# Performance work log

Hardware: AMD Instinct MI355X
Metric: run time of the kernel (lower is better)

## Reference

```python
import jax, jax.numpy as jnp
import numpy as np

N = 50000          # nodes
E = 1_600_000      # edges (avg degree 32)
IN = 128           # in_channels
H = 2              # heads
C = 64             # out_channels per head


def setup_inputs() -> dict:
    key = jax.random.key(0)
    k = jax.random.split(key, 6)
    x = jax.random.normal(k[0], (N, IN), dtype=jnp.float32)
    edge_index = jax.random.randint(k[1], (2, E), 0, N, dtype=jnp.int32)
    W = jax.random.normal(k[2], (IN, H * C), dtype=jnp.float32) / np.sqrt(IN).astype(np.float32)
    att_src = jax.random.normal(k[3], (H, C), dtype=jnp.float32) * 0.1
    att_dst = jax.random.normal(k[4], (H, C), dtype=jnp.float32) * 0.1
    bias = jnp.zeros((C,), dtype=jnp.float32)
    return {"x": x, "W": W, "att_src": att_src, "att_dst": att_dst,
            "bias": bias, "edge_index": edge_index}


def reference(x, W, att_src, att_dst, bias, edge_index):
    Nn = x.shape[0]
    # linear projection per head: [N, H, C]
    h = (x @ W).reshape(Nn, H, C)
    # PyG GATConv default: add self loops
    loops = jnp.arange(Nn, dtype=edge_index.dtype)
    src = jnp.concatenate([edge_index[0], loops])  # [E+N]
    dst = jnp.concatenate([edge_index[1], loops])
    # per-node attention logits: a_src . h, a_dst . h -> [N, H]
    a_s = jnp.sum(h * att_src, axis=-1)
    a_d = jnp.sum(h * att_dst, axis=-1)
    # per-edge score, leaky relu (slope 0.2)
    e = jax.nn.leaky_relu(a_s[src] + a_d[dst], 0.2)  # [E+N, H]
    # softmax over incoming edges per destination node
    emax = jax.lax.stop_gradient(jax.ops.segment_max(e, dst, num_segments=Nn))
    e = jnp.exp(e - emax[dst])
    esum = jax.ops.segment_sum(e, dst, num_segments=Nn)
    alpha = e / (esum[dst] + 1e-16)                  # [E+N, H]
    # attention-weighted message passing: scatter-sum to destinations
    out = jax.ops.segment_sum(h[src] * alpha[:, :, None], dst, num_segments=Nn)  # [N, H, C]
    # concat=False -> mean over heads, then bias
    return out.mean(axis=1) + bias  # [N, C]
```

## Files before the change

### kernel.cpp

```cpp
#include <hip/hip_runtime.h>
#include <hip/hip_bf16.h>


#define NBLK 256
#define TH 512
#define BSH 7
#define BSZ 128
#define MAXBUCK 512
#define PLCAP 8192

typedef __attribute__((ext_vector_type(8))) short bf16x8;
typedef __attribute__((ext_vector_type(4))) float f32x4;

__device__ __forceinline__ ushort f2bf(float f) {
  __hip_bfloat16 b = __float2bfloat16(f);
  union { __hip_bfloat16 b; ushort u; } cv; cv.b = b; return cv.u;
}
__device__ __forceinline__ uint pk2(float a, float b) {
  return (uint)f2bf(a) | ((uint)f2bf(b) << 16);
}

__global__ __launch_bounds__(128) void k_wa(const float* __restrict__ W,
                                            const float* __restrict__ as,
                                            const float* __restrict__ ad,
                                            ushort* __restrict__ wa) {
  const int k = threadIdx.x;
  float s0 = 0.f, s1 = 0.f, d0 = 0.f, d1 = 0.f;
  const float* wr = &W[k * 128];
  for (int c = 0; c < 64; ++c) {
    float w0 = wr[c], w1 = wr[64 + c];
    s0 = fmaf(w0, as[c], s0);
    s1 = fmaf(w1, as[64 + c], s1);
    d0 = fmaf(w0, ad[c], d0);
    d1 = fmaf(w1, ad[64 + c], d1);
  }
  wa[k * 4 + 0] = f2bf(s0);
  wa[k * 4 + 1] = f2bf(s1);
  wa[k * 4 + 2] = f2bf(d0);
  wa[k * 4 + 3] = f2bf(d1);
}

__global__ __launch_bounds__(256) void k_gemm(
    const float* __restrict__ x, const float* __restrict__ W,
    const ushort* __restrict__ wa, __hip_bfloat162* __restrict__ h2,
    float* __restrict__ a_s, float* __restrict__ a_d, int Nn) {
  __shared__ ushort Al[64 * 128];
  char* lb = (char*)Al;
  const int wave = threadIdx.x >> 6;
  const int lane = threadIdx.x & 63;
  const int row0 = blockIdx.x * 64;
  const int l15 = lane & 15;
  const int kb = (lane >> 4) * 8;

  {
    const int t = threadIdx.x;
    const int srow = t >> 2, q = t & 3;
    int gr = row0 + srow; gr = (gr < Nn) ? gr : (Nn - 1);
    const float4* xr = (const float4*)&x[(size_t)gr * 128 + q * 32];
#pragma unroll
    for (int i = 0; i < 4; ++i) {
      float4 v0 = xr[2 * i], v1 = xr[2 * i + 1];
      uint4 w;
      w.x = pk2(v0.x, v0.y); w.y = pk2(v0.z, v0.w);
      w.z = pk2(v1.x, v1.y); w.w = pk2(v1.z, v1.w);
      int byte = srow * 256 + ((q * 64 + i * 16) ^ ((srow & 7) << 4));
      *(uint4*)(lb + byte) = w;
    }
  }

  bf16x8 bfr[2][4];
#pragma unroll
  for (int c = 0; c < 2; ++c) {
#pragma unroll
    for (int ks = 0; ks < 4; ++ks) {
      const float* wp = &W[(ks * 32 + kb) * 128 + wave * 32 + c * 16 + l15];
      union { bf16x8 v; ushort u[8]; } t;
#pragma unroll
      for (int j = 0; j < 8; ++j) t.u[j] = f2bf(wp[j * 128]);
      bfr[c][ks] = t.v;
    }
  }
  bf16x8 wafr[4];
  if (wave == 3) {
#pragma unroll
    for (int ks = 0; ks < 4; ++ks) {
      union { bf16x8 v; ushort u[8]; } t;
#pragma unroll
      for (int j = 0; j < 8; ++j)
        t.u[j] = (l15 < 4) ? wa[(ks * 32 + kb + j) * 4 + l15] : (ushort)0;
      wafr[ks] = t.v;
    }
  }

  __syncthreads();

  f32x4 acc[4][2];
  f32x4 accwa[4];
#pragma unroll
  for (int r = 0; r < 4; ++r) {
    acc[r][0] = (f32x4){0.f, 0.f, 0.f, 0.f};
    acc[r][1] = (f32x4){0.f, 0.f, 0.f, 0.f};
    accwa[r] = (f32x4){0.f, 0.f, 0.f, 0.f};
  }
#pragma unroll
  for (int ks = 0; ks < 4; ++ks) {
    bf16x8 af[4];
#pragma unroll
    for (int r = 0; r < 4; ++r) {
      int row = r * 16 + l15;
      int byte = row * 256 + ((ks * 64 + (lane >> 4) * 16) ^ ((row & 7) << 4));
      uint4 v = *(const uint4*)(lb + byte);
      union { uint4 q; bf16x8 v; } cv; cv.q = v;
      af[r] = cv.v;
    }
#pragma unroll
    for (int r = 0; r < 4; ++r) {
      acc[r][0] = __builtin_amdgcn_mfma_f32_16x16x32_bf16(af[r], bfr[0][ks],
                                                          acc[r][0], 0, 0, 0);
      acc[r][1] = __builtin_amdgcn_mfma_f32_16x16x32_bf16(af[r], bfr[1][ks],
                                                          acc[r][1], 0, 0, 0);
    }
    if (wave == 3) {
#pragma unroll
      for (int r = 0; r < 4; ++r)
        accwa[r] = __builtin_amdgcn_mfma_f32_16x16x32_bf16(af[r], wafr[ks],
                                                           accwa[r], 0, 0, 0);
    }
  }

  ushort* hs = (ushort*)h2;
  const int rbase = (lane >> 4) * 4;
#pragma unroll
  for (int r = 0; r < 4; ++r) {
#pragma unroll
    for (int c = 0; c < 2; ++c) {
      int col = wave * 32 + c * 16 + l15;
#pragma unroll
      for (int i = 0; i < 4; ++i) {
        int grow = row0 + r * 16 + rbase + i;
        if (grow < Nn) hs[(size_t)grow * 128 + col] = f2bf(acc[r][c][i]);
      }
    }
  }
  if (wave == 3) {
#pragma unroll
    for (int r = 0; r < 4; ++r) {
#pragma unroll
      for (int i = 0; i < 4; ++i) {
        int grow = row0 + r * 16 + rbase + i;
        if (grow < Nn) {
          float v = accwa[r][i];
          if (l15 < 2) a_s[grow * 2 + l15] = v;
          else if (l15 < 4) a_d[grow * 2 + (l15 - 2)] = v;
        }
      }
    }
  }
}

__global__ __launch_bounds__(TH) void k_bhist(const int* __restrict__ dst,
                                              int* __restrict__ bhist, int E,
                                              int nbuck, int chunk) {
  __shared__ int hl[MAXBUCK];
  for (int i = threadIdx.x; i < nbuck; i += TH) hl[i] = 0;
  __syncthreads();
  const int s = blockIdx.x * chunk;
  const int e = (s + chunk < E) ? s + chunk : E;
  for (int i = s + threadIdx.x; i < e; i += TH)
    atomicAdd(&hl[dst[i] >> BSH], 1);
  __syncthreads();
  for (int b = threadIdx.x; b < nbuck; b += TH)
    bhist[b * NBLK + blockIdx.x] = hl[b];
}

__global__ __launch_bounds__(NBLK) void k_bscan(const int* __restrict__ bhist,
                                                int* __restrict__ cursors,
                                                int* __restrict__ totals,
                                                int nbuck) {
  __shared__ int tmp[NBLK];
  const int b = blockIdx.x;
  const int t = threadIdx.x;
  const int v = bhist[b * NBLK + t];
  tmp[t] = v;
  __syncthreads();
  for (int d = 1; d < NBLK; d <<= 1) {
    int add = (t >= d) ? tmp[t - d] : 0;
    __syncthreads();
    tmp[t] += add;
    __syncthreads();
  }
  cursors[t * nbuck + b] = tmp[t] - v;
  if (t == NBLK - 1) totals[b] = tmp[t];
}

__global__ __launch_bounds__(MAXBUCK) void k_bbase(const int* __restrict__ totals,
                                                   int* __restrict__ bases,
                                                   int nbuck) {
  __shared__ int tmp[MAXBUCK];
  const int t = threadIdx.x;
  const int v = (t < nbuck) ? totals[t] : 0;
  tmp[t] = v;
  __syncthreads();
  for (int d = 1; d < MAXBUCK; d <<= 1) {
    int add = (t >= d) ? tmp[t - d] : 0;
    __syncthreads();
    tmp[t] += add;
    __syncthreads();
  }
  if (t < nbuck) bases[t] = tmp[t] - v;
  if (t == nbuck - 1) bases[nbuck] = tmp[t];
}

__global__ __launch_bounds__(TH) void k_binsert(
    const int* __restrict__ src, const int* __restrict__ dst,
    const int* __restrict__ cursors, const int* __restrict__ bases,
    int* __restrict__ pairs, int E, int nbuck, int chunk) {
  __shared__ int cur[MAXBUCK];
  for (int i = threadIdx.x; i < nbuck; i += TH)
    cur[i] = cursors[blockIdx.x * nbuck + i] + bases[i];
  __syncthreads();
  const int s = blockIdx.x * chunk;
  const int e = (s + chunk < E) ? s + chunk : E;
  for (int i = s + threadIdx.x; i < e; i += TH) {
    const int d = dst[i];
    const int b = d >> BSH;
    const int p = atomicAdd(&cur[b], 1);
    pairs[p] = ((d & (BSZ - 1)) << 16) | src[i];
  }
}

__global__ __launch_bounds__(256) void k_bucket(
    const int* __restrict__ pairs, const int* __restrict__ bases,
    int* __restrict__ off, int* __restrict__ cnt, int* __restrict__ csr,
    int Nn) {
  __shared__ int pl[PLCAP];
  __shared__ int cl[BSZ];
  __shared__ int tmp[BSZ];
  __shared__ int cu[BSZ];
  const int b = blockIdx.x;
  const int t = threadIdx.x;
  const int n0 = b << BSH;
  if (t < BSZ) cl[t] = 0;
  __syncthreads();
  const int s = bases[b], e = bases[b + 1];
  const int len = e - s;
  const bool fit = (len <= PLCAP);
  if (fit) {
    for (int i = t; i < len; i += 256) {
      int pv = pairs[s + i];
      pl[i] = pv;
      atomicAdd(&cl[pv >> 16], 1);
    }
  } else {
    for (int i = s + t; i < e; i += 256) atomicAdd(&cl[pairs[i] >> 16], 1);
  }
  __syncthreads();
  int v = 0;
  if (t < BSZ) { v = cl[t]; tmp[t] = v; }
  __syncthreads();
  for (int d = 1; d < BSZ; d <<= 1) {
    int add = (t < BSZ && t >= d) ? tmp[t - d] : 0;
    __syncthreads();
    if (t < BSZ) tmp[t] += add;
    __syncthreads();
  }
  if (t < BSZ) {
    const int excl = tmp[t] - v;
    cu[t] = s + excl;
    const int node = n0 + t;
    if (node < Nn) { off[node] = s + excl; cnt[node] = v; }
  }
  __syncthreads();
  if (fit) {
    for (int i = t; i < len; i += 256) {
      const int pv = pl[i];
      const int p = atomicAdd(&cu[pv >> 16], 1);
      csr[p] = pv & 0xffff;
    }
  } else {
    for (int i = s + t; i < e; i += 256) {
      const int pv = pairs[i];
      const int p = atomicAdd(&cu[pv >> 16], 1);
      csr[p] = pv & 0xffff;
    }
  }
}

__device__ __forceinline__ float leaky02(float v) {
  return fmaxf(v, 0.2f * v);
}

__global__ __launch_bounds__(256) void k_aggr(
    const __hip_bfloat162* __restrict__ h2, const float* __restrict__ a_s,
    const float* __restrict__ a_d, const int* __restrict__ off,
    const int* __restrict__ cnt, const int* __restrict__ csr,
    const float* __restrict__ bias, float* __restrict__ out, int Nn) {
  __shared__ uint2 ewA[4][64];
  __shared__ uint2 ewB[4][64];
  const int wave = threadIdx.x >> 6;
  const int lane = threadIdx.x & 63;
  const int d = blockIdx.x * 4 + wave;
  if (d >= Nn) return;
  const int o = off[d];
  const int deg = cnt[d];
  const float2 ad2 = *(const float2*)&a_d[d * 2];
  const char* hb = (const char*)h2;
  const unsigned l4 = lane * 4u;
  const uint4* ebase = (lane < 32) ? (const uint4*)&ewA[wave][0]
                                   : (const uint4*)&ewB[wave][0];

  float acc0 = 0.f, acc1 = 0.f;
  float sw0 = 0.f, sw1 = 0.f;

  for (int c = 0; c < deg; c += 64) {
    int rem = deg - c; if (rem > 64) rem = 64;
    {
      unsigned voff = 0; float w0 = 0.f, w1 = 0.f;
      if (lane < rem) {
        int sl = csr[o + c + lane];
        float2 as2 = *(const float2*)&a_s[sl * 2];
        w0 = __expf(leaky02(as2.x + ad2.x));
        w1 = __expf(leaky02(as2.y + ad2.y));
        voff = (unsigned)sl << 8;
        sw0 += w0; sw1 += w1;
      }
      ewA[wave][lane] = make_uint2(voff, __float_as_uint(w0));
      ewB[wave][lane] = make_uint2(voff, __float_as_uint(w1));
    }
    const int nq = (rem + 1) >> 1;
    int q = 0;
    for (; q + 4 <= nq; q += 4) {
      uint4 p0 = ebase[q + 0];
      uint4 p1 = ebase[q + 1];
      uint4 p2 = ebase[q + 2];
      uint4 p3 = ebase[q + 3];
      __hip_bfloat162 hA0 = *(const __hip_bfloat162*)(hb + (size_t)(p0.x + l4));
      __hip_bfloat162 hB0 = *(const __hip_bfloat162*)(hb + (size_t)(p0.z + l4));
      __hip_bfloat162 hA1 = *(const __hip_bfloat162*)(hb + (size_t)(p1.x + l4));
      __hip_bfloat162 hB1 = *(const __hip_bfloat162*)(hb + (size_t)(p1.z + l4));
      __hip_bfloat162 hA2 = *(const __hip_bfloat162*)(hb + (size_t)(p2.x + l4));
      __hip_bfloat162 hB2 = *(const __hip_bfloat162*)(hb + (size_t)(p2.z + l4));
      __hip_bfloat162 hA3 = *(const __hip_bfloat162*)(hb + (size_t)(p3.x + l4));
      __hip_bfloat162 hB3 = *(const __hip_bfloat162*)(hb + (size_t)(p3.z + l4));
      acc0 = fmaf(__uint_as_float(p0.y), __bfloat162float(hA0.x), acc0);
      acc1 = fmaf(__uint_as_float(p0.y), __bfloat162float(hA0.y), acc1);
      acc0 = fmaf(__uint_as_float(p0.w), __bfloat162float(hB0.x), acc0);
      acc1 = fmaf(__uint_as_float(p0.w), __bfloat162float(hB0.y), acc1);
      acc0 = fmaf(__uint_as_float(p1.y), __bfloat162float(hA1.x), acc0);
      acc1 = fmaf(__uint_as_float(p1.y), __bfloat162float(hA1.y), acc1);
      acc0 = fmaf(__uint_as_float(p1.w), __bfloat162float(hB1.x), acc0);
      acc1 = fmaf(__uint_as_float(p1.w), __bfloat162float(hB1.y), acc1);
      acc0 = fmaf(__uint_as_float(p2.y), __bfloat162float(hA2.x), acc0);
      acc1 = fmaf(__uint_as_float(p2.y), __bfloat162float(hA2.y), acc1);
      acc0 = fmaf(__uint_as_float(p2.w), __bfloat162float(hB2.x), acc0);
      acc1 = fmaf(__uint_as_float(p2.w), __bfloat162float(hB2.y), acc1);
      acc0 = fmaf(__uint_as_float(p3.y), __bfloat162float(hA3.x), acc0);
      acc1 = fmaf(__uint_as_float(p3.y), __bfloat162float(hA3.y), acc1);
      acc0 = fmaf(__uint_as_float(p3.w), __bfloat162float(hB3.x), acc0);
      acc1 = fmaf(__uint_as_float(p3.w), __bfloat162float(hB3.y), acc1);
    }
    for (; q < nq; ++q) {
      uint4 p = ebase[q];
      __hip_bfloat162 hA = *(const __hip_bfloat162*)(hb + (size_t)(p.x + l4));
      __hip_bfloat162 hB = *(const __hip_bfloat162*)(hb + (size_t)(p.z + l4));
      acc0 = fmaf(__uint_as_float(p.y), __bfloat162float(hA.x), acc0);
      acc1 = fmaf(__uint_as_float(p.y), __bfloat162float(hA.y), acc1);
      acc0 = fmaf(__uint_as_float(p.w), __bfloat162float(hB.x), acc0);
      acc1 = fmaf(__uint_as_float(p.w), __bfloat162float(hB.y), acc1);
    }
  }
#pragma unroll
  for (int msk = 1; msk <= 32; msk <<= 1) {
    sw0 += __shfl_xor(sw0, msk, 64);
    sw1 += __shfl_xor(sw1, msk, 64);
  }
  {
    float2 as2 = *(const float2*)&a_s[d * 2];
    float w0 = __expf(leaky02(as2.x + ad2.x));
    float w1 = __expf(leaky02(as2.y + ad2.y));
    sw0 += w0; sw1 += w1;
    float av = (lane < 32) ? w0 : w1;
    __hip_bfloat162 hv = h2[(size_t)d * 64 + lane];
    acc0 = fmaf(av, __bfloat162float(hv.x), acc0);
    acc1 = fmaf(av, __bfloat162float(hv.y), acc1);
  }
  const float invsel = 1.f / (((lane < 32) ? sw0 : sw1) + 1e-16f);
  acc0 *= invsel; acc1 *= invsel;
  float o0 = acc0 + __shfl_down(acc0, 32, 64);
  float o1 = acc1 + __shfl_down(acc1, 32, 64);
  if (lane < 32) {
    int c = lane * 2;
    float2 res = make_float2(0.5f * o0 + bias[c], 0.5f * o1 + bias[c + 1]);
    *(float2*)&out[(size_t)d * 64 + c] = res;
  }
}

extern "C" void kernel_launch(void* const* d_in, const int* in_sizes, int n_in,
                              void* d_out, int out_size, void* d_ws,
                              size_t ws_size, hipStream_t stream) {
  const float* x = (const float*)d_in[0];
  const float* W = (const float*)d_in[1];
  const float* att_s = (const float*)d_in[2];
  const float* att_d = (const float*)d_in[3];
  const float* bias = (const float*)d_in[4];
  const int* ei = (const int*)d_in[5];
  const int Nn = in_sizes[0] / 128;
  const int E = in_sizes[5] / 2;
  const int* src = ei;
  const int* dst = ei + E;
  float* out = (float*)d_out;

  const int nbuck = (Nn + BSZ - 1) >> BSH;
  const int chunk = (E + NBLK - 1) / NBLK;

  __hip_bfloat162* h2 = (__hip_bfloat162*)d_ws;
  float* a_s = (float*)(h2 + (size_t)Nn * 64);
  float* a_d = a_s + (size_t)Nn * 2;
  int* off = (int*)(a_d + (size_t)Nn * 2);
  int* cnt = off + Nn;
  int* bhist = cnt + Nn;
  int* cursors = bhist + (size_t)nbuck * NBLK;
  int* totals = cursors + (size_t)NBLK * nbuck;
  int* bases = totals + nbuck;
  ushort* wa = (ushort*)(bases + nbuck + 1);
  int* pairs = (int*)(wa + 512);
  int* csr = pairs + (size_t)E;

  hipLaunchKernelGGL(k_wa, dim3(1), dim3(128), 0, stream, W, att_s, att_d, wa);
  hipLaunchKernelGGL(k_gemm, dim3((Nn + 63) / 64), dim3(256), 0, stream, x, W,
                     wa, h2, a_s, a_d, Nn);
  hipLaunchKernelGGL(k_bhist, dim3(NBLK), dim3(TH), 0, stream, dst, bhist, E,
                     nbuck, chunk);
  hipLaunchKernelGGL(k_bscan, dim3(nbuck), dim3(NBLK), 0, stream, bhist,
                     cursors, totals, nbuck);
  hipLaunchKernelGGL(k_bbase, dim3(1), dim3(MAXBUCK), 0, stream, totals, bases,
                     nbuck);
  hipLaunchKernelGGL(k_binsert, dim3(NBLK), dim3(TH), 0, stream, src, dst,
                     cursors, bases, pairs, E, nbuck, chunk);
  hipLaunchKernelGGL(k_bucket, dim3(nbuck), dim3(256), 0, stream, pairs, bases,
                     off, cnt, csr, Nn);
  hipLaunchKernelGGL(k_aggr, dim3((Nn + 3) / 4), dim3(256), 0, stream, h2, a_s,
                     a_d, off, cnt, csr, bias, out, Nn);
}
```

Baseline: 117.8 us.

## Fuse GEMM with dst histogram, compute logits in epilogue, two nodes per wave

Merges the projection GEMM and the destination-bucket histogram into one launch, with extra blocks doing the histogram, and drops the separate k_wa kernel. Attention logits are now computed in the GEMM epilogue from fp32 accumulators via shared-memory atomics instead of an extra MFMA on precomputed bf16 weights. The aggregation kernel processes two destination nodes per wave, interleaving their first chunk to expose more independent gathers, and unpacks bf16 with shifts. This removes two launches and raises memory-level parallelism in the gather, at the cost of LDS atomics and more register pressure.

```diff
diff --git a/kernel.cpp b/kernel.cpp
--- a/kernel.cpp
+++ b/kernel.cpp
@@ -19,38 +19,41 @@
 __device__ __forceinline__ uint pk2(float a, float b) {
   return (uint)f2bf(a) | ((uint)f2bf(b) << 16);
 }
-
-__global__ __launch_bounds__(128) void k_wa(const float* __restrict__ W,
-                                            const float* __restrict__ as,
-                                            const float* __restrict__ ad,
-                                            ushort* __restrict__ wa) {
-  const int k = threadIdx.x;
-  float s0 = 0.f, s1 = 0.f, d0 = 0.f, d1 = 0.f;
-  const float* wr = &W[k * 128];
-  for (int c = 0; c < 64; ++c) {
-    float w0 = wr[c], w1 = wr[64 + c];
-    s0 = fmaf(w0, as[c], s0);
-    s1 = fmaf(w1, as[64 + c], s1);
-    d0 = fmaf(w0, ad[c], d0);
-    d1 = fmaf(w1, ad[64 + c], d1);
-  }
-  wa[k * 4 + 0] = f2bf(s0);
-  wa[k * 4 + 1] = f2bf(s1);
-  wa[k * 4 + 2] = f2bf(d0);
-  wa[k * 4 + 3] = f2bf(d1);
-}
-
-__global__ __launch_bounds__(256) void k_gemm(
+__device__ __forceinline__ float leaky02(float v) {
+  return fmaxf(v, 0.2f * v);
+}
+
+__global__ __launch_bounds__(256) void k_mega1(
     const float* __restrict__ x, const float* __restrict__ W,
-    const ushort* __restrict__ wa, __hip_bfloat162* __restrict__ h2,
-    float* __restrict__ a_s, float* __restrict__ a_d, int Nn) {
-  __shared__ ushort Al[64 * 128];
+    const float* __restrict__ att_s, const float* __restrict__ att_d,
+    __hip_bfloat162* __restrict__ h2, float* __restrict__ a_s,
+    float* __restrict__ a_d, int Nn, const int* __restrict__ dst,
+    int* __restrict__ bhist, int E, int nbuck, int chunkE, int ngemm) {
+  __shared__ char smem[64 * 128 * 2 + 64 * 4 * 4];
+  if ((int)blockIdx.x >= ngemm) {
+    int* hl = (int*)smem;
+    const int bb = (int)blockIdx.x - ngemm;
+    for (int i = threadIdx.x; i < nbuck; i += 256) hl[i] = 0;
+    __syncthreads();
+    const int s = bb * chunkE;
+    const int e = (s + chunkE < E) ? s + chunkE : E;
+    for (int i = s + threadIdx.x; i < e; i += 256)
+      atomicAdd(&hl[dst[i] >> BSH], 1);
+    __syncthreads();
+    for (int b = threadIdx.x; b < nbuck; b += 256)
+      bhist[b * NBLK + bb] = hl[b];
+    return;
+  }
+  ushort* Al = (ushort*)smem;
+  float(*asd)[4] = (float(*)[4])(smem + 64 * 128 * 2);
   char* lb = (char*)Al;
   const int wave = threadIdx.x >> 6;
   const int lane = threadIdx.x & 63;
   const int row0 = blockIdx.x * 64;
   const int l15 = lane & 15;
   const int kb = (lane >> 4) * 8;
+
+  ((float*)asd)[threadIdx.x] = 0.f;
 
   {
     const int t = threadIdx.x;
@@ -67,7 +70,6 @@
       *(uint4*)(lb + byte) = w;
     }
   }
-
   bf16x8 bfr[2][4];
 #pragma unroll
   for (int c = 0; c < 2; ++c) {
@@ -80,27 +82,18 @@
       bfr[c][ks] = t.v;
     }
   }
-  bf16x8 wafr[4];
-  if (wave == 3) {
-#pragma unroll
-    for (int ks = 0; ks < 4; ++ks) {
-      union { bf16x8 v; ushort u[8]; } t;
-#pragma unroll
-      for (int j = 0; j < 8; ++j)
-        t.u[j] = (l15 < 4) ? wa[(ks * 32 + kb + j) * 4 + l15] : (ushort)0;
-      wafr[ks] = t.v;
-    }
-  }
+  const int col0 = wave * 32 + l15, col1 = col0 + 16;
+  const float as0c = att_s[col0], as1c = att_s[col1];
+  const float ad0c = att_d[col0], ad1c = att_d[col1];
+  const int head = wave >> 1;
 
   __syncthreads();
 
   f32x4 acc[4][2];
-  f32x4 accwa[4];
 #pragma unroll
   for (int r = 0; r < 4; ++r) {
     acc[r][0] = (f32x4){0.f, 0.f, 0.f, 0.f};
     acc[r][1] = (f32x4){0.f, 0.f, 0.f, 0.f};
-    accwa[r] = (f32x4){0.f, 0.f, 0.f, 0.f};
   }
 #pragma unroll
   for (int ks = 0; ks < 4; ++ks) {
@@ -120,12 +113,6 @@
       acc[r][1] = __builtin_amdgcn_mfma_f32_16x16x32_bf16(af[r], bfr[1][ks],
                                                           acc[r][1], 0, 0, 0);
     }
-    if (wave == 3) {
-#pragma unroll
-      for (int r = 0; r < 4; ++r)
-        accwa[r] = __builtin_amdgcn_mfma_f32_16x16x32_bf16(af[r], wafr[ks],
-                                                           accwa[r], 0, 0, 0);
-    }
   }
 
   ushort* hs = (ushort*)h2;
@@ -133,44 +120,26 @@
 #pragma unroll
   for (int r = 0; r < 4; ++r) {
 #pragma unroll
-    for (int c = 0; c < 2; ++c) {
-      int col = wave * 32 + c * 16 + l15;
-#pragma unroll
-      for (int i = 0; i < 4; ++i) {
-        int grow = row0 + r * 16 + rbase + i;
-        if (grow < Nn) hs[(size_t)grow * 128 + col] = f2bf(acc[r][c][i]);
+    for (int i = 0; i < 4; ++i) {
+      const int lrow = r * 16 + rbase + i;
+      const int grow = row0 + lrow;
+      const float h0 = acc[r][0][i], h1 = acc[r][1][i];
+      if (grow < Nn) {
+        hs[(size_t)grow * 128 + col0] = f2bf(h0);
+        hs[(size_t)grow * 128 + col1] = f2bf(h1);
       }
-    }
-  }
-  if (wave == 3) {
-#pragma unroll
-    for (int r = 0; r < 4; ++r) {
-#pragma unroll
-      for (int i = 0; i < 4; ++i) {
-        int grow = row0 + r * 16 + rbase + i;
-        if (grow < Nn) {
-          float v = accwa[r][i];
-          if (l15 < 2) a_s[grow * 2 + l15] = v;
-          else if (l15 < 4) a_d[grow * 2 + (l15 - 2)] = v;
-        }
-      }
-    }
-  }
-}
-
-__global__ __launch_bounds__(TH) void k_bhist(const int* __restrict__ dst,
-                                              int* __restrict__ bhist, int E,
-                                              int nbuck, int chunk) {
-  __shared__ int hl[MAXBUCK];
-  for (int i = threadIdx.x; i < nbuck; i += TH) hl[i] = 0;
-  __syncthreads();
-  const int s = blockIdx.x * chunk;
-  const int e = (s + chunk < E) ? s + chunk : E;
-  for (int i = s + threadIdx.x; i < e; i += TH)
-    atomicAdd(&hl[dst[i] >> BSH], 1);
-  __syncthreads();
-  for (int b = threadIdx.x; b < nbuck; b += TH)
-    bhist[b * NBLK + blockIdx.x] = hl[b];
+      atomicAdd(&asd[lrow][head], fmaf(h0, as0c, h1 * as1c));
+      atomicAdd(&asd[lrow][2 + head], fmaf(h0, ad0c, h1 * ad1c));
+    }
+  }
+  __syncthreads();
+  if (threadIdx.x < 64) {
+    const int grow = row0 + threadIdx.x;
+    if (grow < Nn) {
+      *(float2*)&a_s[grow * 2] = make_float2(asd[threadIdx.x][0], asd[threadIdx.x][1]);
+      *(float2*)&a_d[grow * 2] = make_float2(asd[threadIdx.x][2], asd[threadIdx.x][3]);
+    }
+  }
 }
 
 __global__ __launch_bounds__(NBLK) void k_bscan(const int* __restrict__ bhist,
@@ -286,8 +255,88 @@
   }
 }
 
-__device__ __forceinline__ float leaky02(float v) {
-  return fmaxf(v, 0.2f * v);
+__device__ __forceinline__ void stage_chunk(
+    const int* __restrict__ csr, const float* __restrict__ a_s, int o,
+    int cbase, int rem, float2 ad2, int lane, uint2* __restrict__ rowA,
+    uint2* __restrict__ rowB, float& swA, float& swB) {
+  uint voff = 0; float w0 = 0.f, w1 = 0.f;
+  if (lane < rem) {
+    int sl = csr[o + cbase + lane];
+    float2 as2 = *(const float2*)&a_s[sl * 2];
+    w0 = __expf(leaky02(as2.x + ad2.x));
+    w1 = __expf(leaky02(as2.y + ad2.y));
+    voff = (uint)sl << 8;
+    swA += w0; swB += w1;
+  }
+  rowA[lane] = make_uint2(voff, __float_as_uint(w0));
+  rowB[lane] = make_uint2(voff, __float_as_uint(w1));
+}
+
+__device__ __forceinline__ void gather8(const uint4* __restrict__ ebase,
+                                        int rem, const char* __restrict__ hb,
+                                        unsigned l4, float& acc0, float& acc1) {
+  const int nq = (rem + 1) >> 1;
+  int q = 0;
+  for (; q + 4 <= nq; q += 4) {
+    uint4 p0 = ebase[q + 0], p1 = ebase[q + 1];
+    uint4 p2 = ebase[q + 2], p3 = ebase[q + 3];
+    uint va0 = *(const uint*)(hb + (size_t)(p0.x + l4));
+    uint vb0 = *(const uint*)(hb + (size_t)(p0.z + l4));
+    uint va1 = *(const uint*)(hb + (size_t)(p1.x + l4));
+    uint vb1 = *(const uint*)(hb + (size_t)(p1.z + l4));
+    uint va2 = *(const uint*)(hb + (size_t)(p2.x + l4));
+    uint vb2 = *(const uint*)(hb + (size_t)(p2.z + l4));
+    uint va3 = *(const uint*)(hb + (size_t)(p3.x + l4));
+    uint vb3 = *(const uint*)(hb + (size_t)(p3.z + l4));
+    acc0 = fmaf(__uint_as_float(p0.y), __uint_as_float(va0 << 16), acc0);
+    acc1 = fmaf(__uint_as_float(p0.y), __uint_as_float(va0 & 0xffff0000u), acc1);
+    acc0 = fmaf(__uint_as_float(p0.w), __uint_as_float(vb0 << 16), acc0);
+    acc1 = fmaf(__uint_as_float(p0.w), __uint_as_float(vb0 & 0xffff0000u), acc1);
+    acc0 = fmaf(__uint_as_float(p1.y), __uint_as_float(va1 << 16), acc0);
+    acc1 = fmaf(__uint_as_float(p1.y), __uint_as_float(va1 & 0xffff0000u), acc1);
+    acc0 = fmaf(__uint_as_float(p1.w), __uint_as_float(vb1 << 16), acc0);
+    acc1 = fmaf(__uint_as_float(p1.w), __uint_as_float(vb1 & 0xffff0000u), acc1);
+    acc0 = fmaf(__uint_as_float(p2.y), __uint_as_float(va2 << 16), acc0);
+    acc1 = fmaf(__uint_as_float(p2.y), __uint_as_float(va2 & 0xffff0000u), acc1);
+    acc0 = fmaf(__uint_as_float(p2.w), __uint_as_float(vb2 << 16), acc0);
+    acc1 = fmaf(__uint_as_float(p2.w), __uint_as_float(vb2 & 0xffff0000u), acc1);
+    acc0 = fmaf(__uint_as_float(p3.y), __uint_as_float(va3 << 16), acc0);
+    acc1 = fmaf(__uint_as_float(p3.y), __uint_as_float(va3 & 0xffff0000u), acc1);
+    acc0 = fmaf(__uint_as_float(p3.w), __uint_as_float(vb3 << 16), acc0);
+    acc1 = fmaf(__uint_as_float(p3.w), __uint_as_float(vb3 & 0xffff0000u), acc1);
+  }
+  for (; q < nq; ++q) {
+    uint4 p = ebase[q];
+    uint va = *(const uint*)(hb + (size_t)(p.x + l4));
+    uint vb = *(const uint*)(hb + (size_t)(p.z + l4));
+    acc0 = fmaf(__uint_as_float(p.y), __uint_as_float(va << 16), acc0);
+    acc1 = fmaf(__uint_as_float(p.y), __uint_as_float(va & 0xffff0000u), acc1);
+    acc0 = fmaf(__uint_as_float(p.w), __uint_as_float(vb << 16), acc0);
+    acc1 = fmaf(__uint_as_float(p.w), __uint_as_float(vb & 0xffff0000u), acc1);
+  }
+}
+
+__device__ __forceinline__ void finish_node(
+    int d, float swA, float swB, float acc0, float acc1, float2 ad2,
+    const float* __restrict__ a_s, const __hip_bfloat162* __restrict__ h2,
+    const float* __restrict__ bias, float* __restrict__ out, int lane) {
+  float2 as2 = *(const float2*)&a_s[d * 2];
+  float w0 = __expf(leaky02(as2.x + ad2.x));
+  float w1 = __expf(leaky02(as2.y + ad2.y));
+  swA += w0; swB += w1;
+  float av = (lane < 32) ? w0 : w1;
+  __hip_bfloat162 hv = h2[(size_t)d * 64 + lane];
+  acc0 = fmaf(av, __bfloat162float(hv.x), acc0);
+  acc1 = fmaf(av, __bfloat162float(hv.y), acc1);
+  float inv = 1.f / (((lane < 32) ? swA : swB) + 1e-16f);
+  acc0 *= inv; acc1 *= inv;
+  float o0 = acc0 + __shfl_down(acc0, 32, 64);
+  float o1 = acc1 + __shfl_down(acc1, 32, 64);
+  if (lane < 32) {
+    int c = lane * 2;
+    *(float2*)&out[(size_t)d * 64 + c] =
+        make_float2(0.5f * o0 + bias[c], 0.5f * o1 + bias[c + 1]);
+  }
 }
 
 __global__ __launch_bounds__(256) void k_aggr(
@@ -295,104 +344,55 @@
     const float* __restrict__ a_d, const int* __restrict__ off,
     const int* __restrict__ cnt, const int* __restrict__ csr,
     const float* __restrict__ bias, float* __restrict__ out, int Nn) {
-  __shared__ uint2 ewA[4][64];
-  __shared__ uint2 ewB[4][64];
+  __shared__ uint2 ewA[8][64];
+  __shared__ uint2 ewB[8][64];
   const int wave = threadIdx.x >> 6;
   const int lane = threadIdx.x & 63;
-  const int d = blockIdx.x * 4 + wave;
-  if (d >= Nn) return;
-  const int o = off[d];
-  const int deg = cnt[d];
-  const float2 ad2 = *(const float2*)&a_d[d * 2];
+  const int d0 = blockIdx.x * 8 + wave * 2;
+  if (d0 >= Nn) return;
+  const int d1 = d0 + 1;
+  const bool has1 = (d1 < Nn);
+  const int o0 = off[d0], n0 = cnt[d0];
+  const int o1 = has1 ? off[d1] : 0;
+  const int n1 = has1 ? cnt[d1] : 0;
+  const float2 ad20 = *(const float2*)&a_d[d0 * 2];
+  const float2 ad21 = has1 ? *(const float2*)&a_d[d1 * 2] : make_float2(0.f, 0.f);
   const char* hb = (const char*)h2;
   const unsigned l4 = lane * 4u;
-  const uint4* ebase = (lane < 32) ? (const uint4*)&ewA[wave][0]
-                                   : (const uint4*)&ewB[wave][0];
-
-  float acc0 = 0.f, acc1 = 0.f;
-  float sw0 = 0.f, sw1 = 0.f;
-
-  for (int c = 0; c < deg; c += 64) {
-    int rem = deg - c; if (rem > 64) rem = 64;
-    {
-      unsigned voff = 0; float w0 = 0.f, w1 = 0.f;
-      if (lane < rem) {
-        int sl = csr[o + c + lane];
-        float2 as2 = *(const float2*)&a_s[sl * 2];
-        w0 = __expf(leaky02(as2.x + ad2.x));
-        w1 = __expf(leaky02(as2.y + ad2.y));
-        voff = (unsigned)sl << 8;
-        sw0 += w0; sw1 += w1;
-      }
-      ewA[wave][lane] = make_uint2(voff, __float_as_uint(w0));
-      ewB[wave][lane] = make_uint2(voff, __float_as_uint(w1));
-    }
-    const int nq = (rem + 1) >> 1;
-    int q = 0;
-    for (; q + 4 <= nq; q += 4) {
-      uint4 p0 = ebase[q + 0];
-      uint4 p1 = ebase[q + 1];
-      uint4 p2 = ebase[q + 2];
-      uint4 p3 = ebase[q + 3];
-      __hip_bfloat162 hA0 = *(const __hip_bfloat162*)(hb + (size_t)(p0.x + l4));
-      __hip_bfloat162 hB0 = *(const __hip_bfloat162*)(hb + (size_t)(p0.z + l4));
-      __hip_bfloat162 hA1 = *(const __hip_bfloat162*)(hb + (size_t)(p1.x + l4));
-      __hip_bfloat162 hB1 = *(const __hip_bfloat162*)(hb + (size_t)(p1.z + l4));
-      __hip_bfloat162 hA2 = *(const __hip_bfloat162*)(hb + (size_t)(p2.x + l4));
-      __hip_bfloat162 hB2 = *(const __hip_bfloat162*)(hb + (size_t)(p2.z + l4));
-      __hip_bfloat162 hA3 = *(const __hip_bfloat162*)(hb + (size_t)(p3.x + l4));
-      __hip_bfloat162 hB3 = *(const __hip_bfloat162*)(hb + (size_t)(p3.z + l4));
-      acc0 = fmaf(__uint_as_float(p0.y), __bfloat162float(hA0.x), acc0);
-      acc1 = fmaf(__uint_as_float(p0.y), __bfloat162float(hA0.y), acc1);
-      acc0 = fmaf(__uint_as_float(p0.w), __bfloat162float(hB0.x), acc0);
-      acc1 = fmaf(__uint_as_float(p0.w), __bfloat162float(hB0.y), acc1);
-      acc0 = fmaf(__uint_as_float(p1.y), __bfloat162float(hA1.x), acc0);
-      acc1 = fmaf(__uint_as_float(p1.y), __bfloat162float(hA1.y), acc1);
-      acc0 = fmaf(__uint_as_float(p1.w), __bfloat162float(hB1.x), acc0);
-      acc1 = fmaf(__uint_as_float(p1.w), __bfloat162float(hB1.y), acc1);
-      acc0 = fmaf(__uint_as_float(p2.y), __bfloat162float(hA2.x), acc0);
-      acc1 = fmaf(__uint_as_float(p2.y), __bfloat162float(hA2.y), acc1);
-      acc0 = fmaf(__uint_as_float(p2.w), __bfloat162float(hB2.x), acc0);
-      acc1 = fmaf(__uint_as_float(p2.w), __bfloat162float(hB2.y), acc1);
-      acc0 = fmaf(__uint_as_float(p3.y), __bfloat162float(hA3.x), acc0);
-      acc1 = fmaf(__uint_as_float(p3.y), __bfloat162float(hA3.y), acc1);
-      acc0 = fmaf(__uint_as_float(p3.w), __bfloat162float(hB3.x), acc0);
-      acc1 = fmaf(__uint_as_float(p3.w), __bfloat162float(hB3.y), acc1);
-    }
-    for (; q < nq; ++q) {
-      uint4 p = ebase[q];
-      __hip_bfloat162 hA = *(const __hip_bfloat162*)(hb + (size_t)(p.x + l4));
-      __hip_bfloat162 hB = *(const __hip_bfloat162*)(hb + (size_t)(p.z + l4));
-      acc0 = fmaf(__uint_as_float(p.y), __bfloat162float(hA.x), acc0);
-      acc1 = fmaf(__uint_as_float(p.y), __bfloat162float(hA.y), acc1);
-      acc0 = fmaf(__uint_as_float(p.w), __bfloat162float(hB.x), acc0);
-      acc1 = fmaf(__uint_as_float(p.w), __bfloat162float(hB.y), acc1);
-    }
-  }
-#pragma unroll
-  for (int msk = 1; msk <= 32; msk <<= 1) {
-    sw0 += __shfl_xor(sw0, msk, 64);
-    sw1 += __shfl_xor(sw1, msk, 64);
-  }
-  {
-    float2 as2 = *(const float2*)&a_s[d * 2];
-    float w0 = __expf(leaky02(as2.x + ad2.x));
-    float w1 = __expf(leaky02(as2.y + ad2.y));
-    sw0 += w0; sw1 += w1;
-    float av = (lane < 32) ? w0 : w1;
-    __hip_bfloat162 hv = h2[(size_t)d * 64 + lane];
-    acc0 = fmaf(av, __bfloat162float(hv.x), acc0);
-    acc1 = fmaf(av, __bfloat162float(hv.y), acc1);
-  }
-  const float invsel = 1.f / (((lane < 32) ? sw0 : sw1) + 1e-16f);
-  acc0 *= invsel; acc1 *= invsel;
-  float o0 = acc0 + __shfl_down(acc0, 32, 64);
-  float o1 = acc1 + __shfl_down(acc1, 32, 64);
-  if (lane < 32) {
-    int c = lane * 2;
-    float2 res = make_float2(0.5f * o0 + bias[c], 0.5f * o1 + bias[c + 1]);
-    *(float2*)&out[(size_t)d * 64 + c] = res;
-  }
+  const int s0 = wave * 2, s1 = wave * 2 + 1;
+  const uint4* eb0 = (lane < 32) ? (const uint4*)&ewA[s0][0]
+                                 : (const uint4*)&ewB[s0][0];
+  const uint4* eb1 = (lane < 32) ? (const uint4*)&ewA[s1][0]
+                                 : (const uint4*)&ewB[s1][0];
+  float acc00 = 0.f, acc01 = 0.f, acc10 = 0.f, acc11 = 0.f;
+  float swA0 = 0.f, swB0 = 0.f, swA1 = 0.f, swB1 = 0.f;
+
+  const int rem0 = (n0 < 64) ? n0 : 64;
+  const int rem1 = (n1 < 64) ? n1 : 64;
+  stage_chunk(csr, a_s, o0, 0, rem0, ad20, lane, ewA[s0], ewB[s0], swA0, swB0);
+  stage_chunk(csr, a_s, o1, 0, rem1, ad21, lane, ewA[s1], ewB[s1], swA1, swB1);
+  gather8(eb0, rem0, hb, l4, acc00, acc01);
+  gather8(eb1, rem1, hb, l4, acc10, acc11);
+  for (int c = 64; c < n0; c += 64) {
+    int rem = n0 - c; if (rem > 64) rem = 64;
+    stage_chunk(csr, a_s, o0, c, rem, ad20, lane, ewA[s0], ewB[s0], swA0, swB0);
+    gather8(eb0, rem, hb, l4, acc00, acc01);
+  }
+  for (int c = 64; c < n1; c += 64) {
+    int rem = n1 - c; if (rem > 64) rem = 64;
+    stage_chunk(csr, a_s, o1, c, rem, ad21, lane, ewA[s1], ewB[s1], swA1, swB1);
+    gather8(eb1, rem, hb, l4, acc10, acc11);
+  }
+#pragma unroll
+  for (int m = 1; m <= 32; m <<= 1) {
+    swA0 += __shfl_xor(swA0, m, 64);
+    swB0 += __shfl_xor(swB0, m, 64);
+    swA1 += __shfl_xor(swA1, m, 64);
+    swB1 += __shfl_xor(swB1, m, 64);
+  }
+  finish_node(d0, swA0, swB0, acc00, acc01, ad20, a_s, h2, bias, out, lane);
+  if (has1)
+    finish_node(d1, swA1, swB1, acc10, acc11, ad21, a_s, h2, bias, out, lane);
 }
 
 extern "C" void kernel_launch(void* const* d_in, const int* in_sizes, int n_in,
@@ -411,7 +411,8 @@
   float* out = (float*)d_out;
 
   const int nbuck = (Nn + BSZ - 1) >> BSH;
-  const int chunk = (E + NBLK - 1) / NBLK;
+  const int chunkI = (E + NBLK - 1) / NBLK;
+  const int ngemm = (Nn + 63) / 64;
 
   __hip_bfloat162* h2 = (__hip_bfloat162*)d_ws;
   float* a_s = (float*)(h2 + (size_t)Nn * 64);
@@ -422,23 +423,20 @@
   int* cursors = bhist + (size_t)nbuck * NBLK;
   int* totals = cursors + (size_t)NBLK * nbuck;
   int* bases = totals + nbuck;
-  ushort* wa = (ushort*)(bases + nbuck + 1);
-  int* pairs = (int*)(wa + 512);
+  int* pairs = bases + nbuck + 1;
   int* csr = pairs + (size_t)E;
 
-  hipLaunchKernelGGL(k_wa, dim3(1), dim3(128), 0, stream, W, att_s, att_d, wa);
-  hipLaunchKernelGGL(k_gemm, dim3((Nn + 63) / 64), dim3(256), 0, stream, x, W,
-                     wa, h2, a_s, a_d, Nn);
-  hipLaunchKernelGGL(k_bhist, dim3(NBLK), dim3(TH), 0, stream, dst, bhist, E,
-                     nbuck, chunk);
+  hipLaunchKernelGGL(k_mega1, dim3(ngemm + NBLK), dim3(256), 0, stream, x, W,
+                     att_s, att_d, h2, a_s, a_d, Nn, dst, bhist, E, nbuck,
+                     chunkI, ngemm);
   hipLaunchKernelGGL(k_bscan, dim3(nbuck), dim3(NBLK), 0, stream, bhist,
                      cursors, totals, nbuck);
   hipLaunchKernelGGL(k_bbase, dim3(1), dim3(MAXBUCK), 0, stream, totals, bases,
                      nbuck);
   hipLaunchKernelGGL(k_binsert, dim3(NBLK), dim3(TH), 0, stream, src, dst,
-                     cursors, bases, pairs, E, nbuck, chunk);
+                     cursors, bases, pairs, E, nbuck, chunkI);
   hipLaunchKernelGGL(k_bucket, dim3(nbuck), dim3(256), 0, stream, pairs, bases,
                      off, cnt, csr, Nn);
-  hipLaunchKernelGGL(k_aggr, dim3((Nn + 3) / 4), dim3(256), 0, stream, h2, a_s,
+  hipLaunchKernelGGL(k_aggr, dim3((Nn + 7) / 8), dim3(256), 0, stream, h2, a_s,
                      a_d, off, cnt, csr, bias, out, Nn);
 }
```

After: 157.4 us. +33.6%, slower.

## Quantize projected node features to int8 with per-row scales for gather

Applied to the files above, without the earlier changes.

The GEMM epilogue now computes a per-row absmax across both heads, quantizes the projected features to int8 with a per-node scale, stages them in LDS and writes coalesced 16-byte rows. The aggregation kernel gathers 2-byte int8 pairs instead of 4-byte bf16 pairs and folds the per-source scale into the attention weight. This halves the bytes of the random neighbor gathers, which likely dominate the aggregation cost. In exchange it adds quantization error beyond bf16 and extra syncs and atomics in the GEMM.

```diff
diff --git a/kernel.cpp b/kernel.cpp
--- a/kernel.cpp
+++ b/kernel.cpp
@@ -18,6 +18,9 @@
 }
 __device__ __forceinline__ uint pk2(float a, float b) {
   return (uint)f2bf(a) | ((uint)f2bf(b) << 16);
+}
+__device__ __forceinline__ float leaky02(float v) {
+  return fmaxf(v, 0.2f * v);
 }
 
 __global__ __launch_bounds__(128) void k_wa(const float* __restrict__ W,
@@ -42,15 +45,19 @@
 
 __global__ __launch_bounds__(256) void k_gemm(
     const float* __restrict__ x, const float* __restrict__ W,
-    const ushort* __restrict__ wa, __hip_bfloat162* __restrict__ h2,
-    float* __restrict__ a_s, float* __restrict__ a_d, int Nn) {
+    const ushort* __restrict__ wa, char* __restrict__ hq,
+    float* __restrict__ scl, float* __restrict__ a_s,
+    float* __restrict__ a_d, int Nn) {
   __shared__ ushort Al[64 * 128];
+  __shared__ uint rmaxu[64];
   char* lb = (char*)Al;
   const int wave = threadIdx.x >> 6;
   const int lane = threadIdx.x & 63;
   const int row0 = blockIdx.x * 64;
   const int l15 = lane & 15;
   const int kb = (lane >> 4) * 8;
+
+  if (threadIdx.x < 64) rmaxu[threadIdx.x] = 0u;
 
   {
     const int t = threadIdx.x;
@@ -128,19 +135,51 @@
     }
   }
 
-  ushort* hs = (ushort*)h2;
   const int rbase = (lane >> 4) * 4;
+  float rm[4][4];
+#pragma unroll
+  for (int r = 0; r < 4; ++r)
+#pragma unroll
+    for (int i = 0; i < 4; ++i)
+      rm[r][i] = fmaxf(fabsf(acc[r][0][i]), fabsf(acc[r][1][i]));
+#pragma unroll
+  for (int m = 1; m <= 8; m <<= 1) {
+#pragma unroll
+    for (int r = 0; r < 4; ++r)
+#pragma unroll
+      for (int i = 0; i < 4; ++i)
+        rm[r][i] = fmaxf(rm[r][i], __shfl_xor(rm[r][i], m, 64));
+  }
+  __syncthreads();
+  if (l15 == 0) {
+#pragma unroll
+    for (int r = 0; r < 4; ++r)
+#pragma unroll
+      for (int i = 0; i < 4; ++i)
+        atomicMax(&rmaxu[r * 16 + rbase + i], __float_as_uint(rm[r][i]));
+  }
+  __syncthreads();
+
+  char* Q = (char*)Al;
 #pragma unroll
   for (int r = 0; r < 4; ++r) {
 #pragma unroll
-    for (int c = 0; c < 2; ++c) {
-      int col = wave * 32 + c * 16 + l15;
-#pragma unroll
-      for (int i = 0; i < 4; ++i) {
-        int grow = row0 + r * 16 + rbase + i;
-        if (grow < Nn) hs[(size_t)grow * 128 + col] = f2bf(acc[r][c][i]);
+    for (int i = 0; i < 4; ++i) {
+      const int lrow = r * 16 + rbase + i;
+      const float inv = 127.f / fmaxf(__uint_as_float(rmaxu[lrow]), 1e-20f);
+#pragma unroll
+      for (int c = 0; c < 2; ++c) {
+        const int col = wave * 32 + c * 16 + l15;
+        int qv = __float2int_rn(acc[r][c][i] * inv);
+        qv = (qv > 127) ? 127 : ((qv < -127) ? -127 : qv);
+        Q[lrow * 128 + col] = (char)qv;
       }
     }
+  }
+  if (threadIdx.x < 64) {
+    const int grow = row0 + threadIdx.x;
+    if (grow < Nn)
+      scl[grow] = __uint_as_float(rmaxu[threadIdx.x]) * (1.f / 127.f);
   }
   if (wave == 3) {
 #pragma unroll
@@ -155,6 +194,16 @@
         }
       }
     }
+  }
+  __syncthreads();
+#pragma unroll
+  for (int k = 0; k < 2; ++k) {
+    const int idx = threadIdx.x * 2 + k;
+    const int row = idx >> 3;
+    const int col = (idx & 7) * 16;
+    uint4 v = *(const uint4*)(Q + row * 128 + col);
+    if (row0 + row < Nn)
+      *(uint4*)&hq[(size_t)(row0 + row) * 128 + col] = v;
   }
 }
 
@@ -286,15 +335,12 @@
   }
 }
 
-__device__ __forceinline__ float leaky02(float v) {
-  return fmaxf(v, 0.2f * v);
-}
-
 __global__ __launch_bounds__(256) void k_aggr(
-    const __hip_bfloat162* __restrict__ h2, const float* __restrict__ a_s,
-    const float* __restrict__ a_d, const int* __restrict__ off,
-    const int* __restrict__ cnt, const int* __restrict__ csr,
-    const float* __restrict__ bias, float* __restrict__ out, int Nn) {
+    const char* __restrict__ hq, const float* __restrict__ scl,
+    const float* __restrict__ a_s, const float* __restrict__ a_d,
+    const int* __restrict__ off, const int* __restrict__ cnt,
+    const int* __restrict__ csr, const float* __restrict__ bias,
+    float* __restrict__ out, int Nn) {
   __shared__ uint2 ewA[4][64];
   __shared__ uint2 ewB[4][64];
   const int wave = threadIdx.x >> 6;
@@ -304,69 +350,72 @@
   const int o = off[d];
   const int deg = cnt[d];
   const float2 ad2 = *(const float2*)&a_d[d * 2];
-  const char* hb = (const char*)h2;
-  const unsigned l4 = lane * 4u;
+  const unsigned l2 = lane * 2u;
   const uint4* ebase = (lane < 32) ? (const uint4*)&ewA[wave][0]
                                    : (const uint4*)&ewB[wave][0];
-
   float acc0 = 0.f, acc1 = 0.f;
   float sw0 = 0.f, sw1 = 0.f;
 
   for (int c = 0; c < deg; c += 64) {
     int rem = deg - c; if (rem > 64) rem = 64;
     {
-      unsigned voff = 0; float w0 = 0.f, w1 = 0.f;
+      unsigned voff = 0; float w0 = 0.f, w1 = 0.f, ws0 = 0.f, ws1 = 0.f;
       if (lane < rem) {
         int sl = csr[o + c + lane];
         float2 as2 = *(const float2*)&a_s[sl * 2];
         w0 = __expf(leaky02(as2.x + ad2.x));
         w1 = __expf(leaky02(as2.y + ad2.y));
-        voff = (unsigned)sl << 8;
+        float s = scl[sl];
+        voff = (unsigned)sl << 7;
         sw0 += w0; sw1 += w1;
+        ws0 = w0 * s; ws1 = w1 * s;
       }
-      ewA[wave][lane] = make_uint2(voff, __float_as_uint(w0));
-      ewB[wave][lane] = make_uint2(voff, __float_as_uint(w1));
+      ewA[wave][lane] = make_uint2(voff, __float_as_uint(ws0));
+      ewB[wave][lane] = make_uint2(voff, __float_as_uint(ws1));
     }
     const int nq = (rem + 1) >> 1;
     int q = 0;
     for (; q + 4 <= nq; q += 4) {
-      uint4 p0 = ebase[q + 0];
-      uint4 p1 = ebase[q + 1];
-      uint4 p2 = ebase[q + 2];
-      uint4 p3 = ebase[q + 3];
-      __hip_bfloat162 hA0 = *(const __hip_bfloat162*)(hb + (size_t)(p0.x + l4));
-      __hip_bfloat162 hB0 = *(const __hip_bfloat162*)(hb + (size_t)(p0.z + l4));
-      __hip_bfloat162 hA1 = *(const __hip_bfloat162*)(hb + (size_t)(p1.x + l4));
-      __hip_bfloat162 hB1 = *(const __hip_bfloat162*)(hb + (size_t)(p1.z + l4));
-      __hip_bfloat162 hA2 = *(const __hip_bfloat162*)(hb + (size_t)(p2.x + l4));
-      __hip_bfloat162 hB2 = *(const __hip_bfloat162*)(hb + (size_t)(p2.z + l4));
-      __hip_bfloat162 hA3 = *(const __hip_bfloat162*)(hb + (size_t)(p3.x + l4));
-      __hip_bfloat162 hB3 = *(const __hip_bfloat162*)(hb + (size_t)(p3.z + l4));
-      acc0 = fmaf(__uint_as_float(p0.y), __bfloat162float(hA0.x), acc0);
-      acc1 = fmaf(__uint_as_float(p0.y), __bfloat162float(hA0.y), acc1);
-      acc0 = fmaf(__uint_as_float(p0.w), __bfloat162float(hB0.x), acc0);
-      acc1 = fmaf(__uint_as_float(p0.w), __bfloat162float(hB0.y), acc1);
-      acc0 = fmaf(__uint_as_float(p1.y), __bfloat162float(hA1.x), acc0);
-      acc1 = fmaf(__uint_as_float(p1.y), __bfloat162float(hA1.y), acc1);
-      acc0 = fmaf(__uint_as_float(p1.w), __bfloat162float(hB1.x), acc0);
-      acc1 = fmaf(__uint_as_float(p1.w), __bfloat162float(hB1.y), acc1);
-      acc0 = fmaf(__uint_as_float(p2.y), __bfloat162float(hA2.x), acc0);
-      acc1 = fmaf(__uint_as_float(p2.y), __bfloat162float(hA2.y), acc1);
-      acc0 = fmaf(__uint_as_float(p2.w), __bfloat162float(hB2.x), acc0);
-      acc1 = fmaf(__uint_as_float(p2.w), __bfloat162float(hB2.y), acc1);
-      acc0 = fmaf(__uint_as_float(p3.y), __bfloat162float(hA3.x), acc0);
-      acc1 = fmaf(__uint_as_float(p3.y), __bfloat162float(hA3.y), acc1);
-      acc0 = fmaf(__uint_as_float(p3.w), __bfloat162float(hB3.x), acc0);
-      acc1 = fmaf(__uint_as_float(p3.w), __bfloat162float(hB3.y), acc1);
+      uint4 p0 = ebase[q + 0], p1 = ebase[q + 1];
+      uint4 p2 = ebase[q + 2], p3 = ebase[q + 3];
+      ushort a0 = *(const ushort*)(hq + (size_t)(p0.x + l2));
+      ushort b0 = *(const ushort*)(hq + (size_t)(p0.z + l2));
+      ushort a1 = *(const ushort*)(hq + (size_t)(p1.x + l2));
+      ushort b1 = *(const ushort*)(hq + (size_t)(p1.z + l2));
+      ushort a2 = *(const ushort*)(hq + (size_t)(p2.x + l2));
+      ushort b2 = *(const ushort*)(hq + (size_t)(p2.z + l2));
+      ushort a3 = *(const ushort*)(hq + (size_t)(p3.x + l2));
+      ushort b3 = *(const ushort*)(hq + (size_t)(p3.z + l2));
+      float wA0 = __uint_as_float(p0.y), wB0 = __uint_as_float(p0.w);
+      float wA1 = __uint_as_float(p1.y), wB1 = __uint_as_float(p1.w);
+      float wA2 = __uint_as_float(p2.y), wB2 = __uint_as_float(p2.w);
+      float wA3 = __uint_as_float(p3.y), wB3 = __uint_as_float(p3.w);
+      acc0 = fmaf(wA0, (float)(signed char)(a0 & 0xff), acc0);
+      acc1 = fmaf(wA0, (float)(signed char)(a0 >> 8), acc1);
+      acc0 = fmaf(wB0, (float)(signed char)(b0 & 0xff), acc0);
+      acc1 = fmaf(wB0, (float)(signed char)(b0 >> 8), acc1);
+      acc0 = fmaf(wA1, (float)(signed char)(a1 & 0xff), acc0);
+      acc1 = fmaf(wA1, (float)(signed char)(a1 >> 8), acc1);
+      acc0 = fmaf(wB1, (float)(signed char)(b1 & 0xff), acc0);
+      acc1 = fmaf(wB1, (float)(signed char)(b1 >> 8), acc1);
+      acc0 = fmaf(wA2, (float)(signed char)(a2 & 0xff), acc0);
+      acc1 = fmaf(wA2, (float)(signed char)(a2 >> 8), acc1);
+      acc0 = fmaf(wB2, (float)(signed char)(b2 & 0xff), acc0);
+      acc1 = fmaf(wB2, (float)(signed char)(b2 >> 8), acc1);
+      acc0 = fmaf(wA3, (float)(signed char)(a3 & 0xff), acc0);
+      acc1 = fmaf(wA3, (float)(signed char)(a3 >> 8), acc1);
+      acc0 = fmaf(wB3, (float)(signed char)(b3 & 0xff), acc0);
+      acc1 = fmaf(wB3, (float)(signed char)(b3 >> 8), acc1);
     }
     for (; q < nq; ++q) {
       uint4 p = ebase[q];
-      __hip_bfloat162 hA = *(const __hip_bfloat162*)(hb + (size_t)(p.x + l4));
-      __hip_bfloat162 hB = *(const __hip_bfloat162*)(hb + (size_t)(p.z + l4));
-      acc0 = fmaf(__uint_as_float(p.y), __bfloat162float(hA.x), acc0);
-      acc1 = fmaf(__uint_as_float(p.y), __bfloat162float(hA.y), acc1);
-      acc0 = fmaf(__uint_as_float(p.w), __bfloat162float(hB.x), acc0);
-      acc1 = fmaf(__uint_as_float(p.w), __bfloat162float(hB.y), acc1);
+      ushort va = *(const ushort*)(hq + (size_t)(p.x + l2));
+      ushort vb = *(const ushort*)(hq + (size_t)(p.z + l2));
+      float wA = __uint_as_float(p.y), wB = __uint_as_float(p.w);
+      acc0 = fmaf(wA, (float)(signed char)(va & 0xff), acc0);
+      acc1 = fmaf(wA, (float)(signed char)(va >> 8), acc1);
+      acc0 = fmaf(wB, (float)(signed char)(vb & 0xff), acc0);
+      acc1 = fmaf(wB, (float)(signed char)(vb >> 8), acc1);
     }
   }
 #pragma unroll
@@ -379,10 +428,10 @@
     float w0 = __expf(leaky02(as2.x + ad2.x));
     float w1 = __expf(leaky02(as2.y + ad2.y));
     sw0 += w0; sw1 += w1;
-    float av = (lane < 32) ? w0 : w1;
-    __hip_bfloat162 hv = h2[(size_t)d * 64 + lane];
-    acc0 = fmaf(av, __bfloat162float(hv.x), acc0);
-    acc1 = fmaf(av, __bfloat162float(hv.y), acc1);
+    float av = ((lane < 32) ? w0 : w1) * scl[d];
+    ushort v = *(const ushort*)(hq + ((size_t)d << 7) + l2);
+    acc0 = fmaf(av, (float)(signed char)(v & 0xff), acc0);
+    acc1 = fmaf(av, (float)(signed char)(v >> 8), acc1);
   }
   const float invsel = 1.f / (((lane < 32) ? sw0 : sw1) + 1e-16f);
   acc0 *= invsel; acc1 *= invsel;
@@ -413,8 +462,9 @@
   const int nbuck = (Nn + BSZ - 1) >> BSH;
   const int chunk = (E + NBLK - 1) / NBLK;
 
-  __hip_bfloat162* h2 = (__hip_bfloat162*)d_ws;
-  float* a_s = (float*)(h2 + (size_t)Nn * 64);
+  char* hq = (char*)d_ws;
+  float* scl = (float*)(hq + (size_t)Nn * 128);
+  float* a_s = scl + Nn;
   float* a_d = a_s + (size_t)Nn * 2;
   int* off = (int*)(a_d + (size_t)Nn * 2);
   int* cnt = off + Nn;
@@ -428,7 +478,7 @@
 
   hipLaunchKernelGGL(k_wa, dim3(1), dim3(128), 0, stream, W, att_s, att_d, wa);
   hipLaunchKernelGGL(k_gemm, dim3((Nn + 63) / 64), dim3(256), 0, stream, x, W,
-                     wa, h2, a_s, a_d, Nn);
+                     wa, hq, scl, a_s, a_d, Nn);
   hipLaunchKernelGGL(k_bhist, dim3(NBLK), dim3(TH), 0, stream, dst, bhist, E,
                      nbuck, chunk);
   hipLaunchKernelGGL(k_bscan, dim3(nbuck), dim3(NBLK), 0, stream, bhist,
@@ -439,6 +489,6 @@
                      cursors, bases, pairs, E, nbuck, chunk);
   hipLaunchKernelGGL(k_bucket, dim3(nbuck), dim3(256), 0, stream, pairs, bases,
                      off, cnt, csr, Nn);
-  hipLaunchKernelGGL(k_aggr, dim3((Nn + 3) / 4), dim3(256), 0, stream, h2, a_s,
-                     a_d, off, cnt, csr, bias, out, Nn);
-}
+  hipLaunchKernelGGL(k_aggr, dim3((Nn + 3) / 4), dim3(256), 0, stream, hq, scl,
+                     a_s, a_d, off, cnt, csr, bias, out, Nn);
+}
```

New measurement: 111.3 us. 5.6% less time.
